# Kernel optimization log

Measured on AMD Instinct MI355X. Metric: run time of the kernel, lower is better.

Reference implementation:

```python
import jax, jax.numpy as jnp
import numpy as np

B_SZ, SEQ = 1, 2048
D_MODEL, D_STATE, D_CONV, EXPAND = 768, 64, 4, 2
D_INNER = EXPAND * D_MODEL            # 1536
HEADDIM = 64
NHEADS = D_INNER // HEADDIM           # 24
CONV_DIM = D_INNER + 2 * D_STATE      # 1664
D_IN_PROJ = 2 * D_INNER + 2 * D_STATE + NHEADS  # 3224
HIDDEN = ((D_MODEL * EXPAND + 127) // 128) * 128  # 1536
EPS = 1e-5


def _ln(x, w, b):
    m = x.mean(-1, keepdims=True)
    v = ((x - m) ** 2).mean(-1, keepdims=True)
    return (x - m) * jax.lax.rsqrt(v + EPS) * w + b


def setup_inputs() -> dict:
    key = jax.random.key(0)
    ks = jax.random.split(key, 8)
    s = 0.02
    return {
        "x": jax.random.normal(ks[0], (B_SZ, SEQ, D_MODEL), jnp.float32),
        "ln1_w": jnp.ones((D_MODEL,), jnp.float32),
        "ln1_b": jnp.zeros((D_MODEL,), jnp.float32),
        "ln2_w": jnp.ones((D_MODEL,), jnp.float32),
        "ln2_b": jnp.zeros((D_MODEL,), jnp.float32),
        "in_proj_w": jax.random.normal(ks[1], (D_IN_PROJ, D_MODEL), jnp.float32) * s,
        "conv_w": jax.random.normal(ks[2], (CONV_DIM, D_CONV), jnp.float32) * s,
        "conv_b": jnp.zeros((CONV_DIM,), jnp.float32),
        "dt_bias": jax.random.normal(ks[3], (NHEADS,), jnp.float32) * 0.1,
        "A_log": jnp.log(jax.random.uniform(ks[4], (NHEADS,), jnp.float32, 1.0, 16.0)),
        "D_skip": jnp.ones((NHEADS,), jnp.float32),
        "ssm_norm_w": jnp.ones((D_INNER,), jnp.float32),
        "out_proj_w": jax.random.normal(ks[5], (D_MODEL, D_INNER), jnp.float32) * s,
        "fc1_w": jax.random.normal(ks[6], (2 * HIDDEN, D_MODEL), jnp.float32) * s,
        "fc2_w": jax.random.normal(ks[7], (D_MODEL, HIDDEN), jnp.float32) * s,
    }


def _block(x, ln1_w, ln1_b, ln2_w, ln2_b, in_proj_w, conv_w, conv_b,
           dt_bias, A_log, D_skip, ssm_norm_w, out_proj_w, fc1_w, fc2_w):
    Bb, L, _ = x.shape
    # --- Mamba2 SSM mixer ---
    h = _ln(x, ln1_w, ln1_b)
    zxbcdt = jnp.einsum('bld,pd->blp', h, in_proj_w)  # (B,L,D_IN_PROJ)
    z = zxbcdt[..., :D_INNER]
    xBC = zxbcdt[..., D_INNER:D_INNER + CONV_DIM]
    dt = zxbcdt[..., D_INNER + CONV_DIM:]             # (B,L,NHEADS)
    # causal depthwise conv1d (kernel D_CONV)
    xp = jnp.pad(xBC, ((0, 0), (D_CONV - 1, 0), (0, 0)))
    xBC = sum(xp[:, k:k + L, :] * conv_w[:, k] for k in range(D_CONV)) + conv_b
    xBC = jax.nn.silu(xBC)
    xs = xBC[..., :D_INNER].reshape(Bb, L, NHEADS, HEADDIM)
    Bm = xBC[..., D_INNER:D_INNER + D_STATE]          # (B,L,N) ngroups=1
    Cm = xBC[..., D_INNER + D_STATE:]                 # (B,L,N)
    dt = jax.nn.softplus(dt + dt_bias)                # (B,L,H)
    dA = jnp.exp(dt * (-jnp.exp(A_log)))              # (B,L,H)
    dtx = dt[..., None] * xs                          # (B,L,H,P)

    def step(hprev, inp):
        dA_t, dtx_t, B_t, C_t = inp
        hn = hprev * dA_t[:, :, None, None] + dtx_t[..., None] * B_t[:, None, None, :]
        return hn, jnp.einsum('bhps,bs->bhp', hn, C_t)

    h0 = jnp.zeros((Bb, NHEADS, HEADDIM, D_STATE), x.dtype)
    _, ys = jax.lax.scan(step, h0, (dA.swapaxes(0, 1), dtx.swapaxes(0, 1),
                                    Bm.swapaxes(0, 1), Cm.swapaxes(0, 1)))
    y = ys.swapaxes(0, 1) + D_skip[None, None, :, None] * xs  # (B,L,H,P)
    y = y.reshape(Bb, L, D_INNER) * jax.nn.silu(z)
    # gated RMSNorm
    y = y * jax.lax.rsqrt((y * y).mean(-1, keepdims=True) + EPS) * ssm_norm_w
    x = x + jnp.einsum('bli,di->bld', y, out_proj_w)
    # --- Gated MLP ---
    h2 = _ln(x, ln2_w, ln2_b)
    f = jnp.einsum('bld,hd->blh', h2, fc1_w)
    f = f[..., :HIDDEN] * jax.nn.silu(f[..., HIDDEN:])
    return x + jnp.einsum('blh,dh->bld', f, fc2_w)


def reference(x, ln1_w, ln1_b, ln2_w, ln2_b, in_proj_w, conv_w, conv_b,
              dt_bias, A_log, D_skip, ssm_norm_w, out_proj_w, fc1_w, fc2_w):
    return _block(x, ln1_w, ln1_b, ln2_w, ln2_b, in_proj_w, conv_w, conv_b,
                  dt_bias, A_log, D_skip, ssm_norm_w, out_proj_w, fc1_w, fc2_w)
```

## Files before the change

### kernel.cpp

```cpp
#include <hip/hip_runtime.h>
#include <math.h>

#define D_MODEL 768
#define SEQ 2048
#define D_STATE 64
#define D_CONV 4
#define D_INNER 1536
#define HEADDIM 64
#define NHEADS 24
#define CONV_DIM 1664
#define D_IN_PROJ 3224
#define HIDDEN 1536
#define EPS 1e-5f
#define NCHUNK 32
#define CHUNK 64

typedef short s16x8 __attribute__((ext_vector_type(8)));
typedef float f32x4 __attribute__((ext_vector_type(4)));

#define SWZ(row, k) (((row) << 6) + ((((k) >> 3) ^ ((row) & 7)) << 3) + ((k) & 7))

__device__ __forceinline__ float silu_f(float x) { return x / (1.f + expf(-x)); }

__device__ __forceinline__ short f2bf(float x) {
  unsigned u = __builtin_bit_cast(unsigned, x);
  unsigned r = (u + 0x7fffu + ((u >> 16) & 1u)) >> 16;
  return (short)r;
}
__device__ __forceinline__ float bf2f(short s) {
  unsigned u = ((unsigned)(unsigned short)s) << 16;
  return __builtin_bit_cast(float, u);
}

__device__ __forceinline__ float block_sum256(float v, float* sdata) {
#pragma unroll
  for (int o = 32; o > 0; o >>= 1) v += __shfl_down(v, o);
  int lane = threadIdx.x & 63, wid = threadIdx.x >> 6;
  __syncthreads();
  if (lane == 0) sdata[wid] = v;
  __syncthreads();
  if (threadIdx.x == 0) sdata[0] = sdata[0] + sdata[1] + sdata[2] + sdata[3];
  __syncthreads();
  return sdata[0];
}

__device__ __forceinline__ void gll16(const short* gsrc, const short* ldst) {
  __builtin_amdgcn_global_load_lds(
      (const __attribute__((address_space(1))) unsigned int*)(unsigned long long)gsrc,
      (__attribute__((address_space(3))) unsigned int*)(unsigned int)(unsigned long long)ldst,
      16, 0, 0);
}

__device__ __forceinline__ void ln_row(const float* __restrict__ xr,
                                       const float* __restrict__ w,
                                       const float* __restrict__ b,
                                       short* __restrict__ orow, float* red) {
  float v[3];
#pragma unroll
  for (int k = 0; k < 3; k++) v[k] = xr[threadIdx.x + k * 256];
  float s = v[0] + v[1] + v[2];
  s = block_sum256(s, red);
  float mean = s * (1.f / 768.f);
  float q = 0.f;
#pragma unroll
  for (int k = 0; k < 3; k++) { float d = v[k] - mean; q += d * d; }
  q = block_sum256(q, red);
  float rstd = rsqrtf(q * (1.f / 768.f) + EPS);
#pragma unroll
  for (int k = 0; k < 3; k++) {
    int i = threadIdx.x + k * 256;
    orow[i] = f2bf((v[k] - mean) * rstd * w[i] + b[i]);
  }
}

__global__ __launch_bounds__(256) void ln_kernel(const float* __restrict__ x,
                                                 const float* __restrict__ w,
                                                 const float* __restrict__ b,
                                                 short* __restrict__ out) {
  __shared__ float red[8];
  int row = blockIdx.x;
  ln_row(x + (size_t)row * D_MODEL, w, b, out + (size_t)row * D_MODEL, red);
}

#define T_WINP (3328 * 768)
#define R_WINP (3224 * 768)
#define T_FC1 (3072 * 768)
#define T_W768 (1536 * 768)
__global__ __launch_bounds__(256) void cast_ln_kernel(
    const float* __restrict__ x, const float* __restrict__ ln1w,
    const float* __restrict__ ln1b, short* __restrict__ hbf,
    const float* __restrict__ Win, const float* __restrict__ Wfc1,
    const float* __restrict__ Wout, const float* __restrict__ Wfc2,
    const float* __restrict__ nrmw,
    short* __restrict__ WA, short* __restrict__ WF1,
    short* __restrict__ WB, short* __restrict__ WC) {
  __shared__ float red[8];
  if (blockIdx.x < SEQ) {
    int row = blockIdx.x;
    ln_row(x + (size_t)row * D_MODEL, ln1w, ln1b, hbf + (size_t)row * D_MODEL, red);
    return;
  }
  int idx = (blockIdx.x - SEQ) * 256 + threadIdx.x;
  if (idx < T_WINP) {
    WA[idx] = (idx < R_WINP) ? f2bf(Win[idx]) : (short)0;
    return;
  }
  idx -= T_WINP;
  if (idx < T_FC1) {
    int np = idx / 768, k = idx % 768;
    int srow = (np & 1) ? (HIDDEN + (np >> 1)) : (np >> 1);
    WF1[idx] = f2bf(Wfc1[(size_t)srow * 768 + k]);
    return;
  }
  idx -= T_FC1;
  if (idx < T_W768) {
    WB[idx] = f2bf(Wout[idx] * nrmw[idx % D_INNER]);
    return;
  }
  idx -= T_W768;
  if (idx < T_W768) WC[idx] = f2bf(Wfc2[idx]);
}

template <int MREP, int NREP, int CHUNKMODE, int OMODE>
__global__ __launch_bounds__(256) void mfma_gemm_bt(const short* __restrict__ A,
                                                    const short* __restrict__ Bw,
                                                    void* __restrict__ Cout,
                                                    const float* __restrict__ res,
                                                    const float* __restrict__ ssqp,
                                                    int GX, int GY, int Nreal, int K) {
  constexpr int BMr = MREP * 32;
  constexpr int BNr = NREP * 32;
  __shared__ short As[BMr * 64];
  __shared__ short Bs[BNr * 64];
  __shared__ float rs_s[BMr];
  int tid = threadIdx.x, w = tid >> 6, l = tid & 63;
  int per8 = gridDim.x >> 3;
  int L = (blockIdx.x & 7) * per8 + (blockIdx.x >> 3);
  int xt, yt;
  if constexpr (CHUNKMODE == 0) { xt = L / GY; yt = L - xt * GY; }
  else                          { yt = L / GX; xt = L - yt * GX; }
  int m0 = yt * BMr, n0 = xt * BNr;
  int wr = (w >> 1) * (MREP * 16), wc = (w & 1) * (NREP * 16);
  f32x4 acc[MREP][NREP] = {};

  if constexpr (OMODE == 3) {
    if (tid < BMr) {
      const float* sp = ssqp + (size_t)(m0 + tid) * NHEADS;
      float s = 0.f;
#pragma unroll
      for (int i = 0; i < NHEADS; i++) s += sp[i];
      rs_s[tid] = rsqrtf(s * (1.f / (float)D_INNER) + EPS);
    }
  }

  for (int kt = 0; kt < K; kt += 64) {
    __syncthreads();
#pragma unroll
    for (int q = 0; q < BMr / 32; q++) {
      int chunk = w * (BMr / 32) + q;
      int rr = chunk * 8 + (l >> 3);
      int gs = (l & 7) ^ (rr & 7);
      gll16(A + (size_t)(m0 + rr) * K + kt + gs * 8, As + chunk * 512);
    }
#pragma unroll
    for (int q = 0; q < BNr / 32; q++) {
      int chunk = w * (BNr / 32) + q;
      int rr = chunk * 8 + (l >> 3);
      int gs = (l & 7) ^ (rr & 7);
      gll16(Bw + (size_t)(n0 + rr) * K + kt + gs * 8, Bs + chunk * 512);
    }
    __syncthreads();
#pragma unroll
    for (int half = 0; half < 2; half++) {
      s16x8 af[MREP], bfr[NREP];
      int kk = half * 32 + (l >> 4) * 8;
#pragma unroll
      for (int mi = 0; mi < MREP; mi++)
        af[mi] = *(const s16x8*)&As[SWZ(wr + mi * 16 + (l & 15), kk)];
#pragma unroll
      for (int nj = 0; nj < NREP; nj++)
        bfr[nj] = *(const s16x8*)&Bs[SWZ(wc + nj * 16 + (l & 15), kk)];
#pragma unroll
      for (int mi = 0; mi < MREP; mi++)
#pragma unroll
        for (int nj = 0; nj < NREP; nj++)
          acc[mi][nj] = __builtin_amdgcn_mfma_f32_16x16x32_bf16(af[mi], bfr[nj],
                                                                acc[mi][nj], 0, 0, 0);
    }
  }
#pragma unroll
  for (int mi = 0; mi < MREP; mi++)
#pragma unroll
    for (int nj = 0; nj < NREP; nj++)
#pragma unroll
      for (int r = 0; r < 4; r++) {
        int lr = wr + mi * 16 + (l >> 4) * 4 + r;
        int mm = m0 + lr;
        int nn = n0 + wc + nj * 16 + (l & 15);
        float v = acc[mi][nj][r];
        if constexpr (OMODE == 0) {
          float* C = (float*)Cout;
          if (nn < Nreal) {
            if (res) v += res[(size_t)mm * Nreal + nn];
            C[(size_t)mm * Nreal + nn] = v;
          }
        } else if constexpr (OMODE == 1) {
          short* C = (short*)Cout;
          if (nn < Nreal) C[(size_t)mm * Nreal + nn] = f2bf(v);
        } else if constexpr (OMODE == 2) {
          float pv = __shfl_xor(v, 1);
          if ((l & 1) == 0) {
            short* g = (short*)Cout;
            g[(size_t)mm * (Nreal >> 1) + (nn >> 1)] = f2bf(v * silu_f(pv));
          }
        } else {
          float* C = (float*)Cout;
          if (nn < Nreal) {
            v = v * rs_s[lr] + res[(size_t)mm * Nreal + nn];
            C[(size_t)mm * Nreal + nn] = v;
          }
        }
      }
}

__global__ __launch_bounds__(256) void conv_pack_kernel(const short* __restrict__ zx,
                                                        const float* __restrict__ cw,
                                                        const float* __restrict__ cb,
                                                        const float* __restrict__ dtb,
                                                        const float* __restrict__ Alog,
                                                        short* __restrict__ xsb,
                                                        short* __restrict__ XTall,
                                                        short* __restrict__ BTg,
                                                        short* __restrict__ BCbf,
                                                        float* __restrict__ dts,
                                                        float* __restrict__ laB) {
  int ct = blockIdx.x, rt = blockIdx.y;
  if (ct == 26) {
    int wv = threadIdx.x >> 6, t = threadIdx.x & 63;
    int gt = rt * 64 + t;
#pragma unroll
    for (int i = 0; i < 6; i++) {
      int h = wv * 6 + i;
      float xv = bf2f(zx[(size_t)gt * D_IN_PROJ + 3200 + h]) + dtb[h];
      float sp = (xv > 20.f) ? xv : log1pf(expf(xv));
      float la = -expf(Alog[h]) * sp;
#pragma unroll
      for (int off = 1; off < 64; off <<= 1) {
        float u = __shfl_up(la, off);
        if (t >= off) la += u;
      }
      dts[gt * NHEADS + h] = sp;
      laB[gt * NHEADS + h] = la;
    }
    return;
  }
  __shared__ float T[64][65];
  int lane = threadIdx.x & 63, grp = threadIdx.x >> 6;
  int c = ct * 64 + lane;
  float4 w4 = *(const float4*)&cw[c * 4];
  float cbv = cb[c];
  int t0 = rt * 64 + grp * 16;
  float vbuf[19];
#pragma unroll
  for (int jj = 0; jj < 19; jj++) {
    int tt = t0 + jj - 3;
    vbuf[jj] = (tt >= 0) ? bf2f(zx[(size_t)tt * D_IN_PROJ + D_INNER + c]) : 0.f;
  }
#pragma unroll
  for (int j = 0; j < 16; j++) {
    float acc = cbv + vbuf[j] * w4.x + vbuf[j + 1] * w4.y +
                vbuf[j + 2] * w4.z + vbuf[j + 3] * w4.w;
    float v = silu_f(acc);
    int row = grp * 16 + j;
    T[row][lane] = v;
    if (ct < 24)
      xsb[(size_t)(rt * 64 + row) * D_INNER + c] = f2bf(v);
    else
      BCbf[(size_t)(rt * 64 + row) * 128 + (ct - 24) * 64 + lane] = f2bf(v);
  }
  __syncthreads();
  if (ct < 24) {
#pragma unroll
    for (int j = 0; j < 16; j++) {
      int cc = grp * 16 + j;
      XTall[(size_t)(ct * 64 + cc) * 2048 + rt * 64 + lane] = f2bf(T[lane][cc]);
    }
  } else if (ct == 24) {
#pragma unroll
    for (int j = 0; j < 16; j++) {
      int cc = grp * 16 + j;
      BTg[(size_t)cc * 2048 + rt * 64 + lane] = f2bf(T[lane][cc]);
    }
  }
}

__global__ __launch_bounds__(256) void ssd_a_kernel(const short* __restrict__ BCbf,
                                                    const short* __restrict__ XTall,
                                                    const short* __restrict__ BTg,
                                                    const float* __restrict__ laB,
                                                    const float* __restrict__ dts,
                                                    short* __restrict__ ylg,
                                                    short* __restrict__ Sbh) {
  __shared__ short Cl[4096], Bl[4096], XTl[4096], BTl[4096], Ml[4096];
  __shared__ float la_s[64], dt_s[64], w_s[64];
  int b = blockIdx.x;
  int c = b / NHEADS, h = b % NHEADS;
  int tid = threadIdx.x, w = tid >> 6, l = tid & 63;

  {
    const short* gC = BCbf + (size_t)(c * 64) * 128 + 64;
    const short* gB = BCbf + (size_t)(c * 64) * 128;
    const short* gX = XTall + (size_t)(h * 64) * 2048 + c * 64;
    const short* gT = BTg + c * 64;
#pragma unroll
    for (int q = 0; q < 2; q++) {
      int row = w * 16 + q * 8 + (l >> 3);
      int ks = (l & 7) ^ (row & 7);
      int lofs = (w * 16 + q * 8) * 64;
      gll16(gC + (size_t)row * 128 + ks * 8, Cl + lofs);
      gll16(gB + (size_t)row * 128 + ks * 8, Bl + lofs);
      gll16(gX + (size_t)row * 2048 + ks * 8, XTl + lofs);
      gll16(gT + (size_t)row * 2048 + ks * 8, BTl + lofs);
    }
  }
  if (tid < 64) {
    la_s[tid] = laB[(c * CHUNK + tid) * NHEADS + h];
    dt_s[tid] = dts[(c * CHUNK + tid) * NHEADS + h];
  }
  __syncthreads();

  f32x4 gacc[4] = {};
#pragma unroll
  for (int kt = 0; kt < 2; kt++) {
    int ar = w * 16 + (l & 15);
    int kk = kt * 32 + (l >> 4) * 8;
    s16x8 af = *(const s16x8*)&Cl[SWZ(ar, kk)];
#pragma unroll
    for (int nj = 0; nj < 4; nj++) {
      s16x8 bf_ = *(const s16x8*)&Bl[SWZ(nj * 16 + (l & 15), kk)];
      gacc[nj] = __builtin_amdgcn_mfma_f32_16x16x32_bf16(af, bf_, gacc[nj], 0, 0, 0);
    }
  }
  if (tid < 64) w_s[tid] = __expf(la_s[63] - la_s[tid]) * dt_s[tid];
#pragma unroll
  for (int nj = 0; nj < 4; nj++)
#pragma unroll
    for (int r = 0; r < 4; r++) {
      int t = w * 16 + (l >> 4) * 4 + r;
      int s = nj * 16 + (l & 15);
      float m = (s <= t) ? gacc[nj][r] * __expf(la_s[t] - la_s[s]) * dt_s[s] : 0.f;
      Ml[SWZ(t, s)] = f2bf(m);
    }
  __syncthreads();
  {
    int s = tid & 63, tg = (tid >> 6) * 16;
#pragma unroll
    for (int j = 0; j < 16; j++) {
      int t = tg + j;
      int a = SWZ(s, t);
      BTl[a] = f2bf(bf2f(BTl[a]) * w_s[t]);
    }
  }
  __syncthreads();

  f32x4 yacc[4] = {};
#pragma unroll
  for (int kt = 0; kt < 2; kt++) {
    int ar = w * 16 + (l & 15);
    int kk = kt * 32 + (l >> 4) * 8;
    s16x8 af = *(const s16x8*)&Ml[SWZ(ar, kk)];
#pragma unroll
    for (int nj = 0; nj < 4; nj++) {
      s16x8 bf_ = *(const s16x8*)&XTl[SWZ(nj * 16 + (l & 15), kk)];
      yacc[nj] = __builtin_amdgcn_mfma_f32_16x16x32_bf16(af, bf_, yacc[nj], 0, 0, 0);
    }
  }
  f32x4 hacc[4] = {};
#pragma unroll
  for (int kt = 0; kt < 2; kt++) {
    int ar = w * 16 + (l & 15);
    int kk = kt * 32 + (l >> 4) * 8;
    s16x8 af = *(const s16x8*)&XTl[SWZ(ar, kk)];
#pragma unroll
    for (int nj = 0; nj < 4; nj++) {
      s16x8 bf_ = *(const s16x8*)&BTl[SWZ(nj * 16 + (l & 15), kk)];
      hacc[nj] = __builtin_amdgcn_mfma_f32_16x16x32_bf16(af, bf_, hacc[nj], 0, 0, 0);
    }
  }
#pragma unroll
  for (int nj = 0; nj < 4; nj++)
#pragma unroll
    for (int r = 0; r < 4; r++) {
      int t = w * 16 + (l >> 4) * 4 + r;
      int p = nj * 16 + (l & 15);
      ylg[(size_t)(c * CHUNK + t) * D_INNER + h * 64 + p] = f2bf(yacc[nj][r]);
      Sbh[((size_t)(c * NHEADS + h) * 64 + t) * 64 + p] = f2bf(hacc[nj][r]);
    }
}

__global__ __launch_bounds__(256) void scan2_kernel(const short* __restrict__ Sbh,
                                                    const float* __restrict__ laB,
                                                    short* __restrict__ Hsbf) {
  int idx = blockIdx.x * 256 + threadIdx.x;
  int hh = idx >> 12;
  int rem = idx & 4095;
  float Sv[NCHUNK];
#pragma unroll
  for (int c = 0; c < NCHUNK; c++)
    Sv[c] = bf2f(Sbh[((size_t)c * NHEADS + hh) * 4096 + rem]);
  float run = 0.f;
#pragma unroll
  for (int c = 0; c < NCHUNK; c++) {
    float P = __expf(laB[(c * CHUNK + CHUNK - 1) * NHEADS + hh]);
    Hsbf[((size_t)c * NHEADS + hh) * 4096 + rem] = f2bf(run);
    run = fmaf(P, run, Sv[c]);
  }
}

__global__ __launch_bounds__(256) void ssd_b_kernel(const short* __restrict__ BCbf,
                                                    const short* __restrict__ Hsbf,
                                                    const float* __restrict__ laB,
                                                    const float* __restrict__ Dsk,
                                                    const short* __restrict__ xsb,
                                                    const short* __restrict__ zx,
                                                    short* __restrict__ ylg,
                                                    float* __restrict__ ssqp) {
  __shared__ short Cl[4096], Hl[4096];
  __shared__ float la_s[64];
  int b = blockIdx.x;
  int c = b / NHEADS, h = b % NHEADS;
  int tid = threadIdx.x, w = tid >> 6, l = tid & 63;
  {
    const short* gC = BCbf + (size_t)(c * 64) * 128 + 64;
    const short* gH = Hsbf + (size_t)(c * NHEADS + h) * 4096;
#pragma unroll
    for (int q = 0; q < 2; q++) {
      int row = w * 16 + q * 8 + (l >> 3);
      int ks = (l & 7) ^ (row & 7);
      int lofs = (w * 16 + q * 8) * 64;
      gll16(gC + (size_t)row * 128 + ks * 8, Cl + lofs);
      gll16(gH + (size_t)row * 64 + ks * 8, Hl + lofs);
    }
  }
  if (tid < 64) la_s[tid] = laB[(c * CHUNK + tid) * NHEADS + h];
  __syncthreads();
  f32x4 acc[4] = {};
#pragma unroll
  for (int kt = 0; kt < 2; kt++) {
    int ar = w * 16 + (l & 15);
    int kk = kt * 32 + (l >> 4) * 8;
    s16x8 af = *(const s16x8*)&Cl[SWZ(ar, kk)];
#pragma unroll
    for (int nj = 0; nj < 4; nj++) {
      s16x8 bf_ = *(const s16x8*)&Hl[SWZ(nj * 16 + (l & 15), kk)];
      acc[nj] = __builtin_amdgcn_mfma_f32_16x16x32_bf16(af, bf_, acc[nj], 0, 0, 0);
    }
  }
  float Dv = Dsk[h];
  float sq[4] = {0.f, 0.f, 0.f, 0.f};
#pragma unroll
  for (int nj = 0; nj < 4; nj++)
#pragma unroll
    for (int r = 0; r < 4; r++) {
      int t = w * 16 + (l >> 4) * 4 + r;
      int p = nj * 16 + (l & 15);
      size_t gt = c * CHUNK + t;
      size_t gi = gt * D_INNER + h * 64 + p;
      float yv = bf2f(ylg[gi]) + acc[nj][r] * __expf(la_s[t]) +
                 Dv * bf2f(xsb[gt * D_INNER + h * 64 + p]);
      float z = bf2f(zx[gt * D_IN_PROJ + h * 64 + p]);
      short gb = f2bf(yv * silu_f(z));
      ylg[gi] = gb;
      float gf = bf2f(gb);
      sq[r] += gf * gf;
    }
#pragma unroll
  for (int r = 0; r < 4; r++) {
    float s = sq[r];
    s += __shfl_xor(s, 1); s += __shfl_xor(s, 2);
    s += __shfl_xor(s, 4); s += __shfl_xor(s, 8);
    if ((l & 15) == 0) {
      int t = w * 16 + (l >> 4) * 4 + r;
      ssqp[(size_t)(c * CHUNK + t) * NHEADS + h] = s;
    }
  }
}

extern "C" void kernel_launch(void* const* d_in, const int* in_sizes, int n_in,
                              void* d_out, int out_size, void* d_ws, size_t ws_size,
                              hipStream_t stream) {
  const float* x     = (const float*)d_in[0];
  const float* ln1w  = (const float*)d_in[1];
  const float* ln1b  = (const float*)d_in[2];
  const float* ln2w  = (const float*)d_in[3];
  const float* ln2b  = (const float*)d_in[4];
  const float* Win   = (const float*)d_in[5];
  const float* convw = (const float*)d_in[6];
  const float* convb = (const float*)d_in[7];
  const float* dtb   = (const float*)d_in[8];
  const float* Alog  = (const float*)d_in[9];
  const float* Dsk   = (const float*)d_in[10];
  const float* nrmw  = (const float*)d_in[11];
  const float* Wout  = (const float*)d_in[12];
  const float* Wfc1  = (const float*)d_in[13];
  const float* Wfc2  = (const float*)d_in[14];
  float* out = (float*)d_out;

  short* zxb   = (short*)d_ws;
  short* xsb   = zxb + 6602752;
  short* ylg   = xsb + 3145728;
  float* Sbf   = (float*)(ylg + 3145728);
  float* dts   = Sbf + 3145728;
  float* laB   = dts + 49152;
  short* hbf   = (short*)(laB + 49152);
  short* WA    = hbf + 1572864;
  short* WF1   = WA + 2555904;
  short* WB    = WF1 + 2359296;
  short* WC    = WB + 1179648;
  short* XTall = WC + 1179648;
  short* BTg   = XTall + 3145728;
  short* BCbf  = BTg + 131072;

  short* Sbh  = (short*)Sbf;
  short* Hsbf = XTall;
  float* x1   = Sbf;
  float* ssqp = dts;
  short* gbf  = zxb;

  cast_ln_kernel<<<SEQ + (T_WINP + T_FC1 + 2 * T_W768 + 255) / 256, 256, 0, stream>>>(
      x, ln1w, ln1b, hbf, Win, Wfc1, Wout, Wfc2, nrmw, WA, WF1, WB, WC);
  mfma_gemm_bt<4, 4, 0, 1><<<26 * 16, 256, 0, stream>>>(hbf, WA, zxb, nullptr, nullptr,
                                                        26, 16, D_IN_PROJ, D_MODEL);
  conv_pack_kernel<<<dim3(27, 32), 256, 0, stream>>>(zxb, convw, convb, dtb, Alog,
                                                     xsb, XTall, BTg, BCbf, dts, laB);
  ssd_a_kernel<<<NCHUNK * NHEADS, 256, 0, stream>>>(BCbf, XTall, BTg, laB, dts, ylg, Sbh);
  scan2_kernel<<<(NHEADS * 4096) / 256, 256, 0, stream>>>(Sbh, laB, Hsbf);
  ssd_b_kernel<<<NCHUNK * NHEADS, 256, 0, stream>>>(BCbf, Hsbf, laB, Dsk, xsb, zxb, ylg, ssqp);
  mfma_gemm_bt<2, 2, 1, 3><<<12 * 32, 256, 0, stream>>>(ylg, WB, x1, x, ssqp,
                                                        12, 32, D_MODEL, D_INNER);
  ln_kernel<<<SEQ, 256, 0, stream>>>(x1, ln2w, ln2b, hbf);
  mfma_gemm_bt<4, 4, 0, 2><<<24 * 16, 256, 0, stream>>>(hbf, WF1, gbf, nullptr, nullptr,
                                                        24, 16, 2 * HIDDEN, D_MODEL);
  mfma_gemm_bt<2, 2, 1, 0><<<12 * 32, 256, 0, stream>>>(gbf, WC, out, x1, nullptr,
                                                        12, 32, D_MODEL, HIDDEN);
}
```

Baseline: 151.4 us.

## Fuse SSD chunk, scan and output kernels into one cooperative kernel

Merges ssd_a, scan2 and ssd_b into a single cooperative kernel. Grid-wide syncs replace the two kernel boundaries, and the C tile stays in LDS across phases. Separately, the bf16 GEMM epilogues now pack two values per 32-bit store using lane shuffles. The aim is to remove launch gaps and redundant reloads, but it relies on all 768 blocks being co-resident (launch bounds of 3 blocks per CU) and adds the cost of grid syncs.

Measured after the change: 346.0 us. 2.29x slower.

```diff
diff --git a/kernel.cpp b/kernel.cpp
--- a/kernel.cpp
+++ b/kernel.cpp
@@ -1,5 +1,8 @@
 #include <hip/hip_runtime.h>
+#include <hip/hip_cooperative_groups.h>
 #include <math.h>
+
+namespace cg = cooperative_groups;
 
 #define D_MODEL 768
 #define SEQ 2048
@@ -30,6 +33,9 @@
 __device__ __forceinline__ float bf2f(short s) {
   unsigned u = ((unsigned)(unsigned short)s) << 16;
   return __builtin_bit_cast(float, u);
+}
+__device__ __forceinline__ unsigned pack2bf(float lo, float hi) {
+  return (unsigned)(unsigned short)f2bf(lo) | ((unsigned)(unsigned short)f2bf(hi) << 16);
 }
 
 __device__ __forceinline__ float block_sum256(float v, float* sdata) {
@@ -205,13 +211,18 @@
             C[(size_t)mm * Nreal + nn] = v;
           }
         } else if constexpr (OMODE == 1) {
-          short* C = (short*)Cout;
-          if (nn < Nreal) C[(size_t)mm * Nreal + nn] = f2bf(v);
+          float pv = __shfl_xor(v, 1);
+          if ((l & 1) == 0 && nn < Nreal) {
+            short* C = (short*)Cout;
+            *(unsigned*)&C[(size_t)mm * Nreal + nn] = pack2bf(v, pv);
+          }
         } else if constexpr (OMODE == 2) {
           float pv = __shfl_xor(v, 1);
-          if ((l & 1) == 0) {
-            short* g = (short*)Cout;
-            g[(size_t)mm * (Nreal >> 1) + (nn >> 1)] = f2bf(v * silu_f(pv));
+          float g = v * silu_f(pv);
+          float g2 = __shfl_xor(g, 2);
+          if ((l & 3) == 0) {
+            short* go = (short*)Cout;
+            *(unsigned*)&go[(size_t)mm * (Nreal >> 1) + (nn >> 1)] = pack2bf(g, g2);
           }
         } else {
           float* C = (float*)Cout;
@@ -294,15 +305,16 @@
   }
 }
 
-__global__ __launch_bounds__(256) void ssd_a_kernel(const short* __restrict__ BCbf,
-                                                    const short* __restrict__ XTall,
-                                                    const short* __restrict__ BTg,
-                                                    const float* __restrict__ laB,
-                                                    const float* __restrict__ dts,
-                                                    short* __restrict__ ylg,
-                                                    short* __restrict__ Sbh) {
+__global__ __launch_bounds__(256, 3) void ssd_fused_kernel(
+    const short* __restrict__ BCbf, const short* __restrict__ XTall,
+    const short* __restrict__ BTg, const float* __restrict__ laB,
+    const float* __restrict__ dts, const float* __restrict__ Dsk,
+    const short* __restrict__ xsb, const short* __restrict__ zx,
+    short* __restrict__ ylg, short* __restrict__ Sbh,
+    short* __restrict__ Hsbf, float* __restrict__ ssqp) {
   __shared__ short Cl[4096], Bl[4096], XTl[4096], BTl[4096], Ml[4096];
   __shared__ float la_s[64], dt_s[64], w_s[64];
+  cg::grid_group grid = cg::this_grid();
   int b = blockIdx.x;
   int c = b / NHEADS, h = b % NHEADS;
   int tid = threadIdx.x, w = tid >> 6, l = tid & 63;
@@ -396,53 +408,39 @@
       ylg[(size_t)(c * CHUNK + t) * D_INNER + h * 64 + p] = f2bf(yacc[nj][r]);
       Sbh[((size_t)(c * NHEADS + h) * 64 + t) * 64 + p] = f2bf(hacc[nj][r]);
     }
-}
-
-__global__ __launch_bounds__(256) void scan2_kernel(const short* __restrict__ Sbh,
-                                                    const float* __restrict__ laB,
-                                                    short* __restrict__ Hsbf) {
-  int idx = blockIdx.x * 256 + threadIdx.x;
-  int hh = idx >> 12;
-  int rem = idx & 4095;
-  float Sv[NCHUNK];
-#pragma unroll
-  for (int c = 0; c < NCHUNK; c++)
-    Sv[c] = bf2f(Sbh[((size_t)c * NHEADS + hh) * 4096 + rem]);
-  float run = 0.f;
-#pragma unroll
-  for (int c = 0; c < NCHUNK; c++) {
-    float P = __expf(laB[(c * CHUNK + CHUNK - 1) * NHEADS + hh]);
-    Hsbf[((size_t)c * NHEADS + hh) * 4096 + rem] = f2bf(run);
-    run = fmaf(P, run, Sv[c]);
-  }
-}
-
-__global__ __launch_bounds__(256) void ssd_b_kernel(const short* __restrict__ BCbf,
-                                                    const short* __restrict__ Hsbf,
-                                                    const float* __restrict__ laB,
-                                                    const float* __restrict__ Dsk,
-                                                    const short* __restrict__ xsb,
-                                                    const short* __restrict__ zx,
-                                                    short* __restrict__ ylg,
-                                                    float* __restrict__ ssqp) {
-  __shared__ short Cl[4096], Hl[4096];
-  __shared__ float la_s[64];
-  int b = blockIdx.x;
-  int c = b / NHEADS, h = b % NHEADS;
-  int tid = threadIdx.x, w = tid >> 6, l = tid & 63;
+
+  grid.sync();
+
   {
-    const short* gC = BCbf + (size_t)(c * 64) * 128 + 64;
+    int idx = b * 256 + tid;
+    if (idx < NHEADS * 4096) {
+      int hh = idx >> 12;
+      int rem = idx & 4095;
+      float Sv[NCHUNK];
+#pragma unroll
+      for (int cc = 0; cc < NCHUNK; cc++)
+        Sv[cc] = bf2f(Sbh[((size_t)cc * NHEADS + hh) * 4096 + rem]);
+      float run = 0.f;
+#pragma unroll
+      for (int cc = 0; cc < NCHUNK; cc++) {
+        float P = __expf(laB[(cc * CHUNK + CHUNK - 1) * NHEADS + hh]);
+        Hsbf[((size_t)cc * NHEADS + hh) * 4096 + rem] = f2bf(run);
+        run = fmaf(P, run, Sv[cc]);
+      }
+    }
+  }
+
+  grid.sync();
+
+  {
     const short* gH = Hsbf + (size_t)(c * NHEADS + h) * 4096;
 #pragma unroll
     for (int q = 0; q < 2; q++) {
       int row = w * 16 + q * 8 + (l >> 3);
       int ks = (l & 7) ^ (row & 7);
-      int lofs = (w * 16 + q * 8) * 64;
-      gll16(gC + (size_t)row * 128 + ks * 8, Cl + lofs);
-      gll16(gH + (size_t)row * 64 + ks * 8, Hl + lofs);
-    }
-  }
-  if (tid < 64) la_s[tid] = laB[(c * CHUNK + tid) * NHEADS + h];
+      gll16(gH + (size_t)row * 64 + ks * 8, Bl + (w * 16 + q * 8) * 64);
+    }
+  }
   __syncthreads();
   f32x4 acc[4] = {};
 #pragma unroll
@@ -452,7 +450,7 @@
     s16x8 af = *(const s16x8*)&Cl[SWZ(ar, kk)];
 #pragma unroll
     for (int nj = 0; nj < 4; nj++) {
-      s16x8 bf_ = *(const s16x8*)&Hl[SWZ(nj * 16 + (l & 15), kk)];
+      s16x8 bf_ = *(const s16x8*)&Bl[SWZ(nj * 16 + (l & 15), kk)];
       acc[nj] = __builtin_amdgcn_mfma_f32_16x16x32_bf16(af, bf_, acc[nj], 0, 0, 0);
     }
   }
@@ -533,9 +531,13 @@
                                                         26, 16, D_IN_PROJ, D_MODEL);
   conv_pack_kernel<<<dim3(27, 32), 256, 0, stream>>>(zxb, convw, convb, dtb, Alog,
                                                      xsb, XTall, BTg, BCbf, dts, laB);
-  ssd_a_kernel<<<NCHUNK * NHEADS, 256, 0, stream>>>(BCbf, XTall, BTg, laB, dts, ylg, Sbh);
-  scan2_kernel<<<(NHEADS * 4096) / 256, 256, 0, stream>>>(Sbh, laB, Hsbf);
-  ssd_b_kernel<<<NCHUNK * NHEADS, 256, 0, stream>>>(BCbf, Hsbf, laB, Dsk, xsb, zxb, ylg, ssqp);
+  {
+    void* args[] = {(void*)&BCbf, (void*)&XTall, (void*)&BTg, (void*)&laB,
+                    (void*)&dts,  (void*)&Dsk,   (void*)&xsb, (void*)&zxb,
+                    (void*)&ylg,  (void*)&Sbh,   (void*)&Hsbf, (void*)&ssqp};
+    hipLaunchCooperativeKernel((void*)ssd_fused_kernel, dim3(NCHUNK * NHEADS),
+                               dim3(256), args, 0, stream);
+  }
   mfma_gemm_bt<2, 2, 1, 3><<<12 * 32, 256, 0, stream>>>(ylg, WB, x1, x, ssqp,
                                                         12, 32, D_MODEL, D_INNER);
   ln_kernel<<<SEQ, 256, 0, stream>>>(x1, ln2w, ln2b, hbf);
```
